# Kernel tuning notes

Hardware: AMD Instinct MI355X
Metric: run time of the kernel (lower is better)

## Reference

```python
import jax, jax.numpy as jnp
import numpy as np

DIM = 256
H = 4
K = 16
R = 4
EPS = 1e-5


def _conv1x1(x, W, b):
    # x: [B, Cin, N, P], W: [Cout, Cin], b: [Cout]
    return jnp.einsum('oc,bcnp->bonp', W, x) + b[None, :, None, None]


def setup_inputs() -> dict:
    key = jax.random.key(0)
    ks = jax.random.split(key, 12)
    B, N = 4, 8192
    s = 1.0 / np.sqrt(DIM)
    inp = {
        'queries': jax.random.normal(ks[0], (B, DIM, N, R), dtype=jnp.float32),
        'feats': jax.random.normal(ks[1], (B, DIM, N, K), dtype=jnp.float32),
        'Wq': jax.random.normal(ks[2], (DIM, DIM), dtype=jnp.float32) * s,
        'bq': jnp.zeros((DIM,), dtype=jnp.float32),
        'Wk': jax.random.normal(ks[3], (DIM, DIM), dtype=jnp.float32) * s,
        'bk': jnp.zeros((DIM,), dtype=jnp.float32),
        'Wv': jax.random.normal(ks[4], (DIM, DIM), dtype=jnp.float32) * s,
        'bv': jnp.zeros((DIM,), dtype=jnp.float32),
        'W1': jax.random.normal(ks[5], (2 * DIM, DIM), dtype=jnp.float32) * s,
        'b1': jnp.zeros((2 * DIM,), dtype=jnp.float32),
        'gamma': jnp.ones((2 * DIM,), dtype=jnp.float32),
        'beta': jnp.zeros((2 * DIM,), dtype=jnp.float32),
        'W2': jax.random.normal(ks[6], (DIM, 2 * DIM), dtype=jnp.float32) * (1.0 / np.sqrt(2 * DIM)),
        'b2': jnp.zeros((DIM,), dtype=jnp.float32),
    }
    return inp


def reference(queries, feats, Wq, bq, Wk, bk, Wv, bv, W1, b1, gamma, beta, W2, b2):
    B, _, N, _ = feats.shape
    d = DIM // H
    queries_iden = queries  # [B, dim, N, r]

    q = _conv1x1(queries, Wq, bq).reshape(B, H, d, N, R)   # [B,h,d,N,r]
    k = _conv1x1(feats, Wk, bk).reshape(B, H, d, N, K)     # [B,h,d,N,K]
    v = _conv1x1(feats, Wv, bv).reshape(B, H, d, N, K)     # [B,h,d,N,K]

    # logits: [B,N,h,r,K]
    logits = jnp.einsum('bhdnr,bhdnk->bnhrk', q, k) * (d ** -0.5)
    soft = jax.nn.softmax(logits, axis=-1)
    # agg: [B,N,h,r,d] -> permute to [B,N,h,d,r] -> [B,N,dim,r] -> [B,dim,N,r]
    agg = jnp.einsum('bnhrk,bhdnk->bnhdr', soft, v)
    agg = agg.reshape(B, N, DIM, R).transpose(0, 2, 1, 3)
    agg = agg + queries_iden

    # FFN: conv1x1 -> BN (training-mode batch stats) -> ReLU -> conv1x1, residual, ReLU
    h1 = _conv1x1(agg, W1, b1)  # [B, 2*dim, N, r]
    mean = jnp.mean(h1, axis=(0, 2, 3), keepdims=True)
    var = jnp.var(h1, axis=(0, 2, 3), keepdims=True)
    h1 = (h1 - mean) * jax.lax.rsqrt(var + EPS)
    h1 = h1 * gamma[None, :, None, None] + beta[None, :, None, None]
    h1 = jax.nn.relu(h1)
    h2 = _conv1x1(h1, W2, b2)
    return jax.nn.relu(h2 + agg)
```

## Files before the change

kernel.cpp:

```cpp
#include <hip/hip_runtime.h>
#include <hip/hip_bf16.h>

#define NB 4
#define NRQ 32768
#define NKF 131072

using u16 = unsigned short;
typedef short bf16x8 __attribute__((ext_vector_type(8)));
typedef float f32x4  __attribute__((ext_vector_type(4)));
typedef u16   u16x8  __attribute__((ext_vector_type(8)));
typedef u16   u16x4  __attribute__((ext_vector_type(4)));
typedef u16   u16x2  __attribute__((ext_vector_type(2)));

#if defined(__has_builtin)
#  if __has_builtin(__builtin_amdgcn_fdot2_f32_bf16)
#    define HAVE_DOT2 1
#  endif
#endif
#ifndef HAVE_DOT2
#  define HAVE_DOT2 0
#endif

#if HAVE_DOT2
typedef __bf16 bfv2 __attribute__((ext_vector_type(2)));
union bpack { bf16x8 v; bfv2 p[4]; };
__device__ __forceinline__ float dot2(bfv2 a, bfv2 b, float c){
  return __builtin_amdgcn_fdot2_f32_bf16(a, b, c, false);
}
#endif
union vpack { bf16x8 v; u16 e[8]; };

__device__ __forceinline__ u16 f2b(float f){
  unsigned u = __float_as_uint(f);
  return (u16)((u + 0x7fffu + ((u >> 16) & 1u)) >> 16);
}
__device__ __forceinline__ float b2f(u16 v){
  return __uint_as_float(((unsigned)v) << 16);
}

#define GLOAD16(g, l) __builtin_amdgcn_global_load_lds( \
    (const __attribute__((address_space(1))) unsigned int*)(g), \
    (__attribute__((address_space(3))) unsigned int*)(l), 16, 0, 0)

__global__ __launch_bounds__(256) void cvtW_k(
    const float* __restrict__ Wk, const float* __restrict__ Wv,
    const float* __restrict__ Wq, const float* __restrict__ W1,
    const float* __restrict__ W2, u16* __restrict__ wT)
{
  long e = ((long)blockIdx.x * 256 + threadIdx.x) * 8;
  const float* src; long off;
  if      (e < 65536)  { src = Wk; off = e; }
  else if (e < 131072) { src = Wv; off = e - 65536; }
  else if (e < 196608) { src = Wq; off = e - 131072; }
  else if (e < 327680) { src = W1; off = e - 196608; }
  else                 { src = W2; off = e - 327680; }
  float4 f0 = *reinterpret_cast<const float4*>(src + off);
  float4 f1 = *reinterpret_cast<const float4*>(src + off + 4);
  u16x8 p;
  p[0]=f2b(f0.x); p[1]=f2b(f0.y); p[2]=f2b(f0.z); p[3]=f2b(f0.w);
  p[4]=f2b(f1.x); p[5]=f2b(f1.y); p[6]=f2b(f1.z); p[7]=f2b(f1.w);
  *reinterpret_cast<u16x8*>(wT + e) = p;
}

__global__ void prep_k(const float* __restrict__ bk, const float* __restrict__ bv,
                       float* __restrict__ bKV, float* __restrict__ stats)
{
  int i = blockIdx.x * 256 + threadIdx.x;
  if (i < 512)       bKV[i] = (i < 256) ? bk[i] : bv[i - 256];
  else               stats[i - 512] = 0.f;
}

__global__ __launch_bounds__(256) void transpose_k(
    const float* __restrict__ in, u16* __restrict__ out,
    int NCtot, long outBatch)
{
  __shared__ u16 sT[64][264];
  const int t = threadIdx.x, b = blockIdx.y;
  const int nr0 = blockIdx.x * 64;
  const int cb = t >> 2, nrq = t & 3;
  const long ib = (long)b * 256 * NCtot + nr0;

  #pragma unroll
  for (int ci = 0; ci < 4; ++ci){
    const int c = cb + ci * 64;
    const float* src = in + ib + (long)c * NCtot + nrq * 16;
    #pragma unroll
    for (int j = 0; j < 4; ++j){
      float4 f = *reinterpret_cast<const float4*>(src + j * 4);
      int nr = nrq * 16 + j * 4;
      sT[nr+0][c] = f2b(f.x); sT[nr+1][c] = f2b(f.y);
      sT[nr+2][c] = f2b(f.z); sT[nr+3][c] = f2b(f.w);
    }
  }
  __syncthreads();
  const int row = t >> 2, qtr = t & 3;
  u16* orow = out + (long)b * outBatch + (long)(nr0 + row) * 256 + qtr * 64;
  #pragma unroll
  for (int i = 0; i < 8; ++i)
    *reinterpret_cast<u16x8*>(orow + i * 8) =
        *reinterpret_cast<const u16x8*>(&sT[row][qtr * 64 + i * 8]);
}

template<int MODE, int KD>
__global__ __launch_bounds__(256) void gemm_k(
    const u16* __restrict__ A, long aBatch, int chTiles,
    const u16* __restrict__ Wb, const float* __restrict__ bias,
    u16* __restrict__ outH, long oBatch, int NCH,
    float* __restrict__ statSum, float* __restrict__ statSq,
    const float* __restrict__ xsc, const float* __restrict__ xsh,
    const u16* __restrict__ residT,
    float* __restrict__ outF, long fBatch)
{
  __shared__ __align__(16) char sA[2][16384];
  __shared__ __align__(16) char sB[2][16384];

  const int t = threadIdx.x, lane = t & 63, wid = t >> 6;
  const int wm = wid >> 1, wn = wid & 1;
  const int b = blockIdx.z;

  const int nwg = gridDim.x, orig = blockIdx.x;
  const int qq = nwg >> 3, rr = nwg & 7, xcd = orig & 7, pos = orig >> 3;
  const int wg = (xcd < rr ? xcd * (qq + 1) : rr * (qq + 1) + (xcd - rr) * qq) + pos;
  const int rowT = wg / chTiles, chT = wg % chTiles;

  const u16* Ab = A + (long)b * aBatch + (long)rowT * 128 * KD;
  const u16* Wt = Wb + (long)chT * 128 * KD;
  const int sub = lane >> 3, kc8 = ((lane & 7) ^ sub) * 8;

  f32x4 acc[4][4];
  #pragma unroll
  for (int i = 0; i < 4; ++i)
    #pragma unroll
    for (int j = 0; j < 4; ++j) acc[i][j] = (f32x4){0.f,0.f,0.f,0.f};

  auto STAGE = [&](int buf, int ks){
    const int k0 = ks * 64;
    if constexpr (MODE == 3){
      const int wrow = t >> 1, whalf = t & 1;
      const u16* arow = Ab + (long)wrow * KD + k0 + whalf * 32;
      #pragma unroll
      for (int i = 0; i < 4; ++i){
        u16x8 v = *reinterpret_cast<const u16x8*>(arow + i * 8);
        const int kb = k0 + whalf*32 + i*8;
        float4 s0 = *reinterpret_cast<const float4*>(xsc + kb);
        float4 s1 = *reinterpret_cast<const float4*>(xsc + kb + 4);
        float4 h0 = *reinterpret_cast<const float4*>(xsh + kb);
        float4 h1 = *reinterpret_cast<const float4*>(xsh + kb + 4);
        u16x8 o;
        o[0]=f2b(fmaxf(b2f(v[0])*s0.x+h0.x,0.f));
        o[1]=f2b(fmaxf(b2f(v[1])*s0.y+h0.y,0.f));
        o[2]=f2b(fmaxf(b2f(v[2])*s0.z+h0.z,0.f));
        o[3]=f2b(fmaxf(b2f(v[3])*s0.w+h0.w,0.f));
        o[4]=f2b(fmaxf(b2f(v[4])*s1.x+h1.x,0.f));
        o[5]=f2b(fmaxf(b2f(v[5])*s1.y+h1.y,0.f));
        o[6]=f2b(fmaxf(b2f(v[6])*s1.z+h1.z,0.f));
        o[7]=f2b(fmaxf(b2f(v[7])*s1.w+h1.w,0.f));
        *reinterpret_cast<u16x8*>(
            sA[buf] + ((wrow*128 + whalf*64 + i*16) ^ ((wrow & 7) << 4))) = o;
      }
      #pragma unroll
      for (int i = 0; i < 4; ++i){
        const int chunk = wid * 4 + i;
        GLOAD16(Wt + (long)(chunk*8 + sub)*KD + k0 + kc8, sB[buf] + chunk*1024);
      }
    } else {
      #pragma unroll
      for (int i = 0; i < 4; ++i){
        const int chunk = wid * 4 + i;
        GLOAD16(Ab + (long)(chunk*8 + sub)*KD + k0 + kc8, sA[buf] + chunk*1024);
        GLOAD16(Wt + (long)(chunk*8 + sub)*KD + k0 + kc8, sB[buf] + chunk*1024);
      }
    }
  };

  constexpr int NT = KD / 64;
  STAGE(0, 0);
  __syncthreads();
  int cur = 0;
  for (int ks = 0; ks < NT; ++ks){
    if (ks + 1 < NT) STAGE(cur ^ 1, ks + 1);
    const char* pA = sA[cur]; const char* pB = sB[cur];
    #pragma unroll
    for (int kk = 0; kk < 2; ++kk){
      bf16x8 af[4], bf[4];
      #pragma unroll
      for (int mi = 0; mi < 4; ++mi){
        int m = wm*64 + mi*16 + (lane & 15);
        af[mi] = *reinterpret_cast<const bf16x8*>(
            pA + ((m*128 + kk*64 + (lane>>4)*16) ^ ((m & 7) << 4)));
      }
      #pragma unroll
      for (int ni = 0; ni < 4; ++ni){
        int c = wn*64 + ni*16 + (lane & 15);
        bf[ni] = *reinterpret_cast<const bf16x8*>(
            pB + ((c*128 + kk*64 + (lane>>4)*16) ^ ((c & 7) << 4)));
      }
      #pragma unroll
      for (int mi = 0; mi < 4; ++mi)
        #pragma unroll
        for (int ni = 0; ni < 4; ++ni)
          acc[mi][ni] = __builtin_amdgcn_mfma_f32_16x16x32_bf16(
              af[mi], bf[ni], acc[mi][ni], 0, 0, 0);
    }
    __syncthreads();
    cur ^= 1;
  }

  int chI[4]; float bv[4];
  #pragma unroll
  for (int ni = 0; ni < 4; ++ni){
    int ch = chT*128 + wn*64 + ni*16 + (lane & 15);
    chI[ni] = ch;
    bv[ni] = bias[ch];
  }
  if (MODE <= 1){
    float s[4] = {0,0,0,0}, sq[4] = {0,0,0,0};
    u16* outb = outH + (long)b * oBatch;
    #pragma unroll
    for (int mi = 0; mi < 4; ++mi){
      #pragma unroll
      for (int j = 0; j < 4; ++j){
        const long row = rowT*128 + wm*64 + mi*16 + (lane>>4)*4 + j;
        #pragma unroll
        for (int ni = 0; ni < 4; ++ni){
          float v = acc[mi][ni][j] + bv[ni];
          outb[row * NCH + chI[ni]] = f2b(v);
          if (MODE == 1){ s[ni] += v; sq[ni] += v * v; }
        }
      }
    }
    if (MODE == 1){
      #pragma unroll
      for (int ni = 0; ni < 4; ++ni){
        s[ni]  += __shfl_xor(s[ni], 16);  s[ni]  += __shfl_xor(s[ni], 32);
        sq[ni] += __shfl_xor(sq[ni], 16); sq[ni] += __shfl_xor(sq[ni], 32);
      }
      if (lane < 16){
        #pragma unroll
        for (int ni = 0; ni < 4; ++ni){
          atomicAdd(&statSum[chI[ni]], s[ni]);
          atomicAdd(&statSq[chI[ni]],  sq[ni]);
        }
      }
    }
  } else {
    const u16* rb = residT + (long)b * ((long)NRQ * 256);
    #pragma unroll
    for (int mi = 0; mi < 4; ++mi){
      const int nr0 = rowT*128 + wm*64 + mi*16 + (lane>>4)*4;
      #pragma unroll
      for (int ni = 0; ni < 4; ++ni){
        float4 o;
        o.x = fmaxf(acc[mi][ni][0] + bv[ni] + b2f(rb[(long)(nr0+0)*256 + chI[ni]]), 0.f);
        o.y = fmaxf(acc[mi][ni][1] + bv[ni] + b2f(rb[(long)(nr0+1)*256 + chI[ni]]), 0.f);
        o.z = fmaxf(acc[mi][ni][2] + bv[ni] + b2f(rb[(long)(nr0+2)*256 + chI[ni]]), 0.f);
        o.w = fmaxf(acc[mi][ni][3] + bv[ni] + b2f(rb[(long)(nr0+3)*256 + chI[ni]]), 0.f);
        *reinterpret_cast<float4*>(outF + (long)b*fBatch + (long)chI[ni]*NRQ + nr0) = o;
      }
    }
  }
}

__global__ __launch_bounds__(512, 4) void kvattn_k(
    const float* __restrict__ feats, const u16* __restrict__ wKV,
    const float* __restrict__ bKV, const u16* __restrict__ qT,
    const u16* __restrict__ qrT, u16* __restrict__ aggT)
{
  __shared__ __align__(16) char LDS[73728];
  char*  sAg = LDS;
  char*  sW  = LDS + 8192;
  char*  sK  = LDS;
  char*  sV  = LDS + 33792;
  float* sSf = (float*)(LDS + 67072);

  const int t = threadIdx.x, lane = t & 63, wid = t >> 6;
  const int wr = wid >> 2, wc = wid & 3;
  const int b = blockIdx.y;
  const long row0 = (long)blockIdx.x * 64;

  const int chL = t >> 4, nq = t & 15;
  const float* fbase = feats + (long)b * 256 * NKF + row0 + nq * 4;

  auto STAGEW = [&](int buf, int ks){
    const int k0 = ks * 32;
    #pragma unroll
    for (int i = 0; i < 4; ++i){
      const int cw = wid * 4 + i;
      const int ch = cw * 16 + (lane >> 2), jd = lane & 3;
      GLOAD16(wKV + (long)ch * 256 + k0 + ((jd ^ ((ch >> 1) & 3)) * 8),
              sW + buf * 32768 + cw * 1024);
    }
  };
  auto WRITEA = [&](int buf, float4 f){
    #pragma unroll
    for (int i = 0; i < 4; ++i){
      const int r = nq * 4 + i;
      const int byte = buf*4096 + r*64
                     + (((chL>>3) ^ ((r>>2)&3)) << 4) + (chL & 7)*2;
      float e = (i == 0) ? f.x : (i == 1) ? f.y : (i == 2) ? f.z : f.w;
      *reinterpret_cast<u16*>(sAg + byte) = f2b(e);
    }
  };

  f32x4 acc[2][8];
  #pragma unroll
  for (int i = 0; i < 2; ++i)
    #pragma unroll
    for (int j = 0; j < 8; ++j) acc[i][j] = (f32x4){0.f,0.f,0.f,0.f};

  {
    float4 a0 = *reinterpret_cast<const float4*>(fbase + (long)chL * NKF);
    STAGEW(0, 0);
    WRITEA(0, a0);
  }
  __syncthreads();
  int cur = 0;
  for (int ks = 0; ks < 8; ++ks){
    float4 an;
    if (ks < 7){
      an = *reinterpret_cast<const float4*>(fbase + (long)((ks+1)*32 + chL) * NKF);
      STAGEW(cur ^ 1, ks + 1);
    }
    const char* pA = sAg + cur * 4096;
    const char* pW = sW  + cur * 32768;
    bf16x8 af[2];
    #pragma unroll
    for (int mi = 0; mi < 2; ++mi){
      const int m = wr*32 + mi*16 + (lane & 15);
      af[mi] = *reinterpret_cast<const bf16x8*>(
          pA + m*64 + (((lane>>4) ^ ((m>>2)&3)) * 16));
    }
    #pragma unroll
    for (int ni = 0; ni < 8; ++ni){
      const int ch = wc*128 + ni*16 + (lane & 15);
      bf16x8 bf = *reinterpret_cast<const bf16x8*>(
          pW + ch*64 + (((lane>>4) ^ ((ch>>1)&3)) * 16));
      acc[0][ni] = __builtin_amdgcn_mfma_f32_16x16x32_bf16(af[0], bf, acc[0][ni], 0,0,0);
      acc[1][ni] = __builtin_amdgcn_mfma_f32_16x16x32_bf16(af[1], bf, acc[1][ni], 0,0,0);
    }
    if (ks < 7) WRITEA(cur ^ 1, an);
    __syncthreads();
    cur ^= 1;
  }

  {
    float bv[8];
    #pragma unroll
    for (int ni = 0; ni < 8; ++ni) bv[ni] = bKV[wc*128 + ni*16 + (lane & 15)];
    if (wc < 2){
      #pragma unroll
      for (int mi = 0; mi < 2; ++mi){
        const int p2 = wr*2 + mi;
        #pragma unroll
        for (int ni = 0; ni < 8; ++ni){
          const int ch = wc*128 + ni*16 + (lane & 15);
          #pragma unroll
          for (int j = 0; j < 4; ++j){
            const int kk2 = (lane>>4)*4 + j;
            *reinterpret_cast<u16*>(
                sK + (p2*16 + kk2)*528 + ((ch*2) ^ ((kk2 & 7) << 4))) =
                f2b(acc[mi][ni][j] + bv[ni]);
          }
        }
      }
    } else {
      #pragma unroll
      for (int mi = 0; mi < 2; ++mi){
        const int p2 = wr*2 + mi;
        #pragma unroll
        for (int ni = 0; ni < 8; ++ni){
          const int cv = (wc-2)*128 + ni*16 + (lane & 15);
          #pragma unroll
          for (int j = 0; j < 4; ++j){
            const int kk2 = (lane>>4)*4 + j;
            *reinterpret_cast<u16*>(sV + (p2*16 + kk2)*520 + cv*2) =
                f2b(acc[mi][ni][j] + bv[ni]);
          }
        }
      }
    }
  }
  __syncthreads();

  const int p = wid & 3, rh = wid >> 2;
  const int nqg = blockIdx.x * 4 + p;
  {
    const int h = lane >> 4, kk = lane & 15;
    const u16* qb = qT + ((long)b*NRQ + (long)nqg*4 + rh*2)*256 + h*64;
    const char* kr = sK + (p*16 + kk)*528;
    float l0 = 0.f, l1 = 0.f;
#if HAVE_DOT2
    #pragma unroll
    for (int d8 = 0; d8 < 8; ++d8){
      bpack K8, Q0, Q1;
      K8.v = *reinterpret_cast<const bf16x8*>(
          kr + ((h*128 + d8*16) ^ ((kk & 7) << 4)));
      Q0.v = *reinterpret_cast<const bf16x8*>(qb + d8*8);
      Q1.v = *reinterpret_cast<const bf16x8*>(qb + 256 + d8*8);
      #pragma unroll
      for (int pi = 0; pi < 4; ++pi){
        l0 = dot2(K8.p[pi], Q0.p[pi], l0);
        l1 = dot2(K8.p[pi], Q1.p[pi], l1);
      }
    }
#else
    #pragma unroll
    for (int d8 = 0; d8 < 8; ++d8){
      vpack K8, Q0, Q1;
      K8.v = *reinterpret_cast<const bf16x8*>(
          kr + ((h*128 + d8*16) ^ ((kk & 7) << 4)));
      Q0.v = *reinterpret_cast<const bf16x8*>(qb + d8*8);
      Q1.v = *reinterpret_cast<const bf16x8*>(qb + 256 + d8*8);
      #pragma unroll
      for (int e = 0; e < 8; ++e){
        float kf = b2f(K8.e[e]);
        l0 = fmaf(kf, b2f(Q0.e[e]), l0);
        l1 = fmaf(kf, b2f(Q1.e[e]), l1);
      }
    }
#endif
    float pr[2]; float lv[2] = {l0, l1};
    #pragma unroll
    for (int r = 0; r < 2; ++r){
      float x = lv[r] * 0.125f;
      float m = x;
      #pragma unroll
      for (int off = 1; off < 16; off <<= 1) m = fmaxf(m, __shfl_xor(m, off));
      float e = __expf(x - m);
      float ssum = e;
      #pragma unroll
      for (int off = 1; off < 16; off <<= 1) ssum += __shfl_xor(ssum, off);
      pr[r] = e / ssum;
    }
    *reinterpret_cast<float2*>(sSf + (p*4 + h)*68 + kk*4 + rh*2) =
        make_float2(pr[0], pr[1]);
  }
  __syncthreads();

  {
    const int c0 = rh*128 + lane*2;
    const int h = c0 >> 6;
    const char* vrow = sV + (p*16)*520;
    const float* ss = sSf + (p*4 + h)*68;
    float a[4][2] = {};
    #pragma unroll
    for (int kk = 0; kk < 16; ++kk){
      u16x2 vv = *reinterpret_cast<const u16x2*>(vrow + kk*520 + c0*2);
      float4 sv = *reinterpret_cast<const float4*>(ss + kk*4);
      float v0 = b2f(vv[0]), v1 = b2f(vv[1]);
      a[0][0] += sv.x*v0; a[0][1] += sv.x*v1;
      a[1][0] += sv.y*v0; a[1][1] += sv.y*v1;
      a[2][0] += sv.z*v0; a[2][1] += sv.z*v1;
      a[3][0] += sv.w*v0; a[3][1] += sv.w*v1;
    }
    const u16* rq = qrT + ((long)b*NRQ + (long)nqg*4)*256 + c0;
    u16* ob = aggT + ((long)b*NRQ + (long)nqg*4)*256 + c0;
    #pragma unroll
    for (int r = 0; r < 4; ++r){
      u16x2 q2 = *reinterpret_cast<const u16x2*>(rq + r*256);
      u16x2 pk;
      pk[0] = f2b(a[r][0] + b2f(q2[0]));
      pk[1] = f2b(a[r][1] + b2f(q2[1]));
      *reinterpret_cast<u16x2*>(ob + r*256) = pk;
    }
  }
}

__global__ void finalize_k(const float* __restrict__ st,
                           const float* __restrict__ gamma,
                           const float* __restrict__ beta,
                           float* __restrict__ out)
{
  int o = blockIdx.x*256 + threadIdx.x;
  const float inv = 1.f / 131072.f;
  float mean = st[o] * inv;
  float var  = st[512 + o] * inv - mean*mean;
  float sc   = gamma[o] * rsqrtf(var + 1e-5f);
  out[o]       = sc;
  out[512 + o] = beta[o] - mean * sc;
}

extern "C" void kernel_launch(void* const* d_in, const int* in_sizes, int n_in,
                              void* d_out, int out_size, void* d_ws, size_t ws_size,
                              hipStream_t stream)
{
  (void)in_sizes; (void)n_in; (void)out_size; (void)ws_size;
  const float* queries = (const float*)d_in[0];
  const float* feats   = (const float*)d_in[1];
  const float* Wq = (const float*)d_in[2];
  const float* bq = (const float*)d_in[3];
  const float* Wk = (const float*)d_in[4];
  const float* bk = (const float*)d_in[5];
  const float* Wv = (const float*)d_in[6];
  const float* bv = (const float*)d_in[7];
  const float* W1 = (const float*)d_in[8];
  const float* b1 = (const float*)d_in[9];
  const float* gamma = (const float*)d_in[10];
  const float* beta  = (const float*)d_in[11];
  const float* W2 = (const float*)d_in[12];
  const float* b2 = (const float*)d_in[13];

  char* ws = (char*)d_ws;
  u16*   h1T   = (u16*)ws;
  u16*   qrT   = (u16*)(ws + 134217728L);
  u16*   qT    = (u16*)(ws + 201326592L);
  u16*   aggT  = (u16*)(ws + 268435456L);
  float* stats = (float*)(ws + 335544320L);
  float* scale = stats + 1024;
  float* shift = stats + 1536;
  u16*   wT    = (u16*)(ws + 335552512L);
  u16*   wKV   = wT;
  u16*   wQ    = wT + 131072;
  u16*   wW1   = wT + 196608;
  u16*   wW2   = wT + 327680;
  float* bKV   = (float*)(wT + 458752);

  cvtW_k<<<dim3(224), 256, 0, stream>>>(Wk, Wv, Wq, W1, W2, wT);
  prep_k<<<dim3(6), 256, 0, stream>>>(bk, bv, bKV, stats);

  transpose_k<<<dim3(NRQ/64, NB), 256, 0, stream>>>(queries, qrT, NRQ, (long)NRQ*256);

  gemm_k<0, 256><<<dim3(512, 1, NB), 256, 0, stream>>>(
      qrT, (long)NRQ*256, 2, wQ, bq,
      qT, (long)NRQ*256, 256, nullptr, nullptr, nullptr, nullptr,
      nullptr, nullptr, 0);

  kvattn_k<<<dim3(NKF/64, NB), 512, 0, stream>>>(feats, wKV, bKV, qT, qrT, aggT);

  gemm_k<1, 256><<<dim3(1024, 1, NB), 256, 0, stream>>>(
      aggT, (long)NRQ*256, 4, wW1, b1,
      h1T, (long)NRQ*512, 512, stats, stats + 512, nullptr, nullptr,
      nullptr, nullptr, 0);

  finalize_k<<<dim3(2), 256, 0, stream>>>(stats, gamma, beta, scale);

  gemm_k<3, 512><<<dim3(512, 1, NB), 256, 0, stream>>>(
      h1T, (long)NRQ*512, 2, wW2, b2,
      nullptr, 0, 256, nullptr, nullptr, scale, shift,
      aggT, (float*)d_out, (long)256*NRQ);
}
```

Baseline: 649.3 us.

## Deepen feats prefetch in kvattn, pad A tile, merge prep kernel into cvtW

The kvattn GEMM loop now prefetches feats two k-steps ahead into alternating registers and replaces __syncthreads with explicit waitcnt plus s_barrier, with sched_barrier and setprio around the MFMAs. The A tile switches from XOR swizzle to a padded 72-byte row stride, which slightly enlarges LDS. The residual qrT loads are hoisted before a barrier, the prep kernel is folded into cvtW_k to remove one launch, and f2b now uses the HIP bf16 intrinsic. The aim is to hide global load latency and cut launch overhead, at the cost of more registers and LDS, which may lower occupancy.

```diff
diff --git a/kernel.cpp b/kernel.cpp
--- a/kernel.cpp
+++ b/kernel.cpp
@@ -31,8 +31,8 @@
 union vpack { bf16x8 v; u16 e[8]; };
 
 __device__ __forceinline__ u16 f2b(float f){
-  unsigned u = __float_as_uint(f);
-  return (u16)((u + 0x7fffu + ((u >> 16) & 1u)) >> 16);
+  __hip_bfloat16 h = __float2bfloat16(f);
+  return *reinterpret_cast<u16*>(&h);
 }
 __device__ __forceinline__ float b2f(u16 v){
   return __uint_as_float(((unsigned)v) << 16);
@@ -45,8 +45,16 @@
 __global__ __launch_bounds__(256) void cvtW_k(
     const float* __restrict__ Wk, const float* __restrict__ Wv,
     const float* __restrict__ Wq, const float* __restrict__ W1,
-    const float* __restrict__ W2, u16* __restrict__ wT)
+    const float* __restrict__ W2, u16* __restrict__ wT,
+    const float* __restrict__ bk, const float* __restrict__ bv,
+    float* __restrict__ bKV, float* __restrict__ stats)
 {
+  if (blockIdx.x >= 224){
+    int i = (blockIdx.x - 224) * 256 + threadIdx.x;
+    if (i < 512)       bKV[i] = (i < 256) ? bk[i] : bv[i - 256];
+    else if (i < 1536) stats[i - 512] = 0.f;
+    return;
+  }
   long e = ((long)blockIdx.x * 256 + threadIdx.x) * 8;
   const float* src; long off;
   if      (e < 65536)  { src = Wk; off = e; }
@@ -60,14 +68,6 @@
   p[0]=f2b(f0.x); p[1]=f2b(f0.y); p[2]=f2b(f0.z); p[3]=f2b(f0.w);
   p[4]=f2b(f1.x); p[5]=f2b(f1.y); p[6]=f2b(f1.z); p[7]=f2b(f1.w);
   *reinterpret_cast<u16x8*>(wT + e) = p;
-}
-
-__global__ void prep_k(const float* __restrict__ bk, const float* __restrict__ bv,
-                       float* __restrict__ bKV, float* __restrict__ stats)
-{
-  int i = blockIdx.x * 256 + threadIdx.x;
-  if (i < 512)       bKV[i] = (i < 256) ? bk[i] : bv[i - 256];
-  else               stats[i - 512] = 0.f;
 }
 
 __global__ __launch_bounds__(256) void transpose_k(
@@ -213,7 +213,7 @@
     chI[ni] = ch;
     bv[ni] = bias[ch];
   }
-  if (MODE <= 1){
+  if (MODE != 3){
     float s[4] = {0,0,0,0}, sq[4] = {0,0,0,0};
     u16* outb = outH + (long)b * oBatch;
     #pragma unroll
@@ -266,9 +266,9 @@
     const float* __restrict__ bKV, const u16* __restrict__ qT,
     const u16* __restrict__ qrT, u16* __restrict__ aggT)
 {
-  __shared__ __align__(16) char LDS[73728];
+  __shared__ __align__(16) char LDS[74752];
   char*  sAg = LDS;
-  char*  sW  = LDS + 8192;
+  char*  sW  = LDS + 9216;
   char*  sK  = LDS;
   char*  sV  = LDS + 33792;
   float* sSf = (float*)(LDS + 67072);
@@ -295,10 +295,8 @@
     #pragma unroll
     for (int i = 0; i < 4; ++i){
       const int r = nq * 4 + i;
-      const int byte = buf*4096 + r*64
-                     + (((chL>>3) ^ ((r>>2)&3)) << 4) + (chL & 7)*2;
       float e = (i == 0) ? f.x : (i == 1) ? f.y : (i == 2) ? f.z : f.w;
-      *reinterpret_cast<u16*>(sAg + byte) = f2b(e);
+      *reinterpret_cast<u16*>(sAg + buf*4608 + r*72 + chL*2) = f2b(e);
     }
   };
 
@@ -308,38 +306,51 @@
     #pragma unroll
     for (int j = 0; j < 8; ++j) acc[i][j] = (f32x4){0.f,0.f,0.f,0.f};
 
+  float4 aReg0, aReg1;
   {
-    float4 a0 = *reinterpret_cast<const float4*>(fbase + (long)chL * NKF);
+    aReg0 = *reinterpret_cast<const float4*>(fbase + (long)chL * NKF);
+    aReg1 = *reinterpret_cast<const float4*>(fbase + (long)(32 + chL) * NKF);
     STAGEW(0, 0);
-    WRITEA(0, a0);
+    WRITEA(0, aReg0);
   }
   __syncthreads();
+
   int cur = 0;
+  const int jq = lane >> 4;
+  #pragma unroll
   for (int ks = 0; ks < 8; ++ks){
-    float4 an;
-    if (ks < 7){
-      an = *reinterpret_cast<const float4*>(fbase + (long)((ks+1)*32 + chL) * NKF);
-      STAGEW(cur ^ 1, ks + 1);
-    }
-    const char* pA = sAg + cur * 4096;
+    if (ks < 7) STAGEW(cur ^ 1, ks + 1);
+    __builtin_amdgcn_sched_barrier(0);
+    if (ks < 6){
+      float4 f = *reinterpret_cast<const float4*>(
+          fbase + (long)((ks + 2) * 32 + chL) * NKF);
+      if ((ks & 1) == 0) aReg0 = f; else aReg1 = f;
+    }
+    const char* pA = sAg + cur * 4608;
     const char* pW = sW  + cur * 32768;
     bf16x8 af[2];
     #pragma unroll
     for (int mi = 0; mi < 2; ++mi){
       const int m = wr*32 + mi*16 + (lane & 15);
-      af[mi] = *reinterpret_cast<const bf16x8*>(
-          pA + m*64 + (((lane>>4) ^ ((m>>2)&3)) * 16));
-    }
+      af[mi] = *reinterpret_cast<const bf16x8*>(pA + m*72 + jq*16);
+    }
+    __builtin_amdgcn_s_setprio(1);
     #pragma unroll
     for (int ni = 0; ni < 8; ++ni){
       const int ch = wc*128 + ni*16 + (lane & 15);
       bf16x8 bf = *reinterpret_cast<const bf16x8*>(
-          pW + ch*64 + (((lane>>4) ^ ((ch>>1)&3)) * 16));
+          pW + ch*64 + (((jq ^ ((ch>>1)&3)) * 16)));
       acc[0][ni] = __builtin_amdgcn_mfma_f32_16x16x32_bf16(af[0], bf, acc[0][ni], 0,0,0);
       acc[1][ni] = __builtin_amdgcn_mfma_f32_16x16x32_bf16(af[1], bf, acc[1][ni], 0,0,0);
     }
-    if (ks < 7) WRITEA(cur ^ 1, an);
-    __syncthreads();
+    __builtin_amdgcn_s_setprio(0);
+    if (ks < 7) WRITEA(cur ^ 1, ((ks + 1) & 1) == 0 ? aReg0 : aReg1);
+    if (ks < 6){
+      asm volatile("s_waitcnt vmcnt(1) lgkmcnt(0)" ::: "memory");
+    } else {
+      asm volatile("s_waitcnt vmcnt(0) lgkmcnt(0)" ::: "memory");
+    }
+    __builtin_amdgcn_s_barrier();
     cur ^= 1;
   }
 
@@ -380,10 +391,19 @@
       }
     }
   }
-  __syncthreads();
 
   const int p = wid & 3, rh = wid >> 2;
   const int nqg = blockIdx.x * 4 + p;
+  const int c0 = rh*128 + lane*2;
+  u16x2 rq[4];
+  {
+    const u16* rqp = qrT + ((long)b*NRQ + (long)nqg*4)*256 + c0;
+    #pragma unroll
+    for (int r = 0; r < 4; ++r)
+      rq[r] = *reinterpret_cast<const u16x2*>(rqp + r*256);
+  }
+  __syncthreads();
+
   {
     const int h = lane >> 4, kk = lane & 15;
     const u16* qb = qT + ((long)b*NRQ + (long)nqg*4 + rh*2)*256 + h*64;
@@ -432,13 +452,12 @@
       for (int off = 1; off < 16; off <<= 1) ssum += __shfl_xor(ssum, off);
       pr[r] = e / ssum;
     }
-    *reinterpret_cast<float2*>(sSf + (p*4 + h)*68 + kk*4 + rh*2) =
+    *reinterpret_cast<float2*>(sSf + (p*4 + (lane>>4))*68 + (lane&15)*4 + rh*2) =
         make_float2(pr[0], pr[1]);
   }
   __syncthreads();
 
   {
-    const int c0 = rh*128 + lane*2;
     const int h = c0 >> 6;
     const char* vrow = sV + (p*16)*520;
     const float* ss = sSf + (p*4 + h)*68;
@@ -453,14 +472,12 @@
       a[2][0] += sv.z*v0; a[2][1] += sv.z*v1;
       a[3][0] += sv.w*v0; a[3][1] += sv.w*v1;
     }
-    const u16* rq = qrT + ((long)b*NRQ + (long)nqg*4)*256 + c0;
     u16* ob = aggT + ((long)b*NRQ + (long)nqg*4)*256 + c0;
     #pragma unroll
     for (int r = 0; r < 4; ++r){
-      u16x2 q2 = *reinterpret_cast<const u16x2*>(rq + r*256);
       u16x2 pk;
-      pk[0] = f2b(a[r][0] + b2f(q2[0]));
-      pk[1] = f2b(a[r][1] + b2f(q2[1]));
+      pk[0] = f2b(a[r][0] + b2f(rq[r][0]));
+      pk[1] = f2b(a[r][1] + b2f(rq[r][1]));
       *reinterpret_cast<u16x2*>(ob + r*256) = pk;
     }
   }
@@ -515,8 +532,8 @@
   u16*   wW2   = wT + 327680;
   float* bKV   = (float*)(wT + 458752);
 
-  cvtW_k<<<dim3(224), 256, 0, stream>>>(Wk, Wv, Wq, W1, W2, wT);
-  prep_k<<<dim3(6), 256, 0, stream>>>(bk, bv, bKV, stats);
+  cvtW_k<<<dim3(230), 256, 0, stream>>>(Wk, Wv, Wq, W1, W2, wT,
+                                        bk, bv, bKV, stats);
 
   transpose_k<<<dim3(NRQ/64, NB), 256, 0, stream>>>(queries, qrT, NRQ, (long)NRQ*256);
 
@@ -525,7 +542,8 @@
       qT, (long)NRQ*256, 256, nullptr, nullptr, nullptr, nullptr,
       nullptr, nullptr, 0);
 
-  kvattn_k<<<dim3(NKF/64, NB), 512, 0, stream>>>(feats, wKV, bKV, qT, qrT, aggT);
+  kvattn_k<<<dim3(NKF/64, NB), 512, 0, stream>>>(
+      feats, wKV, bKV, qT, qrT, aggT);
 
   gemm_k<1, 256><<<dim3(1024, 1, NB), 256, 0, stream>>>(
       aggT, (long)NRQ*256, 4, wW1, b1,
```

After: 663.1 us. +2.1%, slower.
